# Optimization experiments

Hardware: AMD Instinct MI355X
Metric: run time of the kernel (lower is better)

The kernel has to match this reference:

```python
import jax, jax.numpy as jnp
import numpy as np

EMBD = 256
HEAD = 4
HD = EMBD // HEAD  # 64
EPS = 1e-5


def setup_inputs() -> dict:
    key = jax.random.key(0)
    ks = jax.random.split(key, 12)
    s = lambda fan_in: 1.0 / np.sqrt(fan_in)
    return {
        "x": jax.random.normal(ks[0], (16, 1024, EMBD), dtype=jnp.float32),
        # attention params (stored as [in, out])
        "qkv_w": jax.random.uniform(ks[1], (EMBD, 3 * EMBD), jnp.float32, -s(EMBD), s(EMBD)),
        "qkv_b": jax.random.uniform(ks[2], (3 * EMBD,), jnp.float32, -s(EMBD), s(EMBD)),
        "out_w": jax.random.uniform(ks[3], (EMBD, EMBD), jnp.float32, -s(EMBD), s(EMBD)),
        "out_b": jax.random.uniform(ks[4], (EMBD,), jnp.float32, -s(EMBD), s(EMBD)),
        # MLP params
        "fc_w": jax.random.uniform(ks[5], (EMBD, 4 * EMBD), jnp.float32, -s(EMBD), s(EMBD)),
        "fc_b": jax.random.uniform(ks[6], (4 * EMBD,), jnp.float32, -s(EMBD), s(EMBD)),
        "proj_w": jax.random.uniform(ks[7], (4 * EMBD, EMBD), jnp.float32, -s(4 * EMBD), s(4 * EMBD)),
        "proj_b": jax.random.uniform(ks[8], (EMBD,), jnp.float32, -s(4 * EMBD), s(4 * EMBD)),
        # LayerNorm params
        "ln1_g": jnp.ones((EMBD,), jnp.float32),
        "ln1_b": jnp.zeros((EMBD,), jnp.float32),
        "ln2_g": jnp.ones((EMBD,), jnp.float32),
        "ln2_b": jnp.zeros((EMBD,), jnp.float32),
    }


def layer_norm(x, g, b):
    mu = jnp.mean(x, axis=-1, keepdims=True)
    var = jnp.mean(jnp.square(x - mu), axis=-1, keepdims=True)
    return (x - mu) * jax.lax.rsqrt(var + EPS) * g + b


def block_forward(x, qkv_w, qkv_b, out_w, out_b, fc_w, fc_b, proj_w, proj_b,
                  ln1_g, ln1_b, ln2_g, ln2_b):
    B, S, E = x.shape
    # --- attention branch ---
    h = layer_norm(x, ln1_g, ln1_b)
    qkv = h @ qkv_w + qkv_b                       # [B,S,3E]
    q, k, v = jnp.split(qkv, 3, axis=-1)
    q = q.reshape(B, S, HEAD, HD).transpose(0, 2, 1, 3)  # [B,H,S,D]
    k = k.reshape(B, S, HEAD, HD).transpose(0, 2, 1, 3)
    v = v.reshape(B, S, HEAD, HD).transpose(0, 2, 1, 3)
    att = jnp.einsum('bhqd,bhkd->bhqk', q, k) / jnp.sqrt(jnp.float32(HD))
    causal = jnp.tril(jnp.ones((S, S), dtype=bool))
    att = jnp.where(causal, att, -jnp.inf)
    att = jax.nn.softmax(att, axis=-1)
    o = jnp.einsum('bhqk,bhkd->bhqd', att, v)     # [B,H,S,D]
    o = o.transpose(0, 2, 1, 3).reshape(B, S, E)
    x = x + o @ out_w + out_b
    # --- MLP branch (dropout inactive at eval) ---
    h = layer_norm(x, ln2_g, ln2_b)
    h = jax.nn.relu(h @ fc_w + fc_b)
    x = x + h @ proj_w + proj_b
    return x


def reference(x, qkv_w, qkv_b, out_w, out_b, fc_w, fc_b, proj_w, proj_b,
              ln1_g, ln1_b, ln2_g, ln2_b):
    return block_forward(x, qkv_w, qkv_b, out_w, out_b, fc_w, fc_b,
                         proj_w, proj_b, ln1_g, ln1_b, ln2_g, ln2_b)
```

## Files before the change

### kernel.cpp

```cpp
#include <hip/hip_runtime.h>
#include <cstdint>


using f32x4  = __attribute__((ext_vector_type(4))) float;
using f32x16 = __attribute__((ext_vector_type(16))) float;
using s16x8  = __attribute__((ext_vector_type(8))) short;
using s16x4  = __attribute__((ext_vector_type(4))) short;

__device__ inline short f2bf(float f) {
    union { float f; unsigned u; } v{f};
    unsigned r = (v.u + 0x7FFFu + ((v.u >> 16) & 1u)) >> 16;
    return (short)r;
}

__device__ inline int cvt_pk_bf16(float lo, float hi) {
    int d;
    asm("v_cvt_pk_bf16_f32 %0, %1, %2" : "=v"(d) : "v"(lo), "v"(hi));
    return d;
}
__device__ inline void swap32(int& a, int& b) {
    asm("v_permlane32_swap_b32 %0, %1" : "+v"(a), "+v"(b));
}
__device__ inline void swap16(int& a, int& b) {
    asm("v_permlane16_swap_b32 %0, %1" : "+v"(a), "+v"(b));
}

__device__ inline void gload16(const void* g, void* l) {
    __builtin_amdgcn_global_load_lds(
        (const __attribute__((address_space(1))) void*)g,
        (__attribute__((address_space(3))) void*)l, 16, 0, 0);
}

__global__ __launch_bounds__(256) void prep_kernel(
    const float* __restrict__ qkv_w, const float* __restrict__ out_w,
    const float* __restrict__ fc_w,  const float* __restrict__ proj_w,
    short* __restrict__ wt_qkv, short* __restrict__ wt_out,
    short* __restrict__ wt_fc,  short* __restrict__ wt_proj,
    const float* __restrict__ x, const float* __restrict__ ln1_g,
    const float* __restrict__ ln1_b, short* __restrict__ hout)
{
    __shared__ short T[64][65];
    int id  = blockIdx.x;
    int tid = threadIdx.x;

    if (id < 192) {
        const float* W; short* Wt; int K, N, nt, kt;
        if (id < 48)       { W = qkv_w;  Wt = wt_qkv;  K = 256;  N = 768;  nt = id % 12;        kt = id / 12; }
        else if (id < 64)  { W = out_w;  Wt = wt_out;  K = 256;  N = 256;  nt = (id - 48) & 3;  kt = (id - 48) >> 2; }
        else if (id < 128) { W = fc_w;   Wt = wt_fc;   K = 256;  N = 1024; nt = (id - 64) & 15; kt = (id - 64) >> 4; }
        else               { W = proj_w; Wt = wt_proj; K = 1024; N = 256;  nt = (id - 128) & 3; kt = (id - 128) >> 2; }
        int n0 = nt * 64, k0 = kt * 64;
        int r = tid >> 2, c = (tid & 3) << 4;
        const float* src = W + (size_t)(k0 + r) * N + n0 + c;
#pragma unroll
        for (int u = 0; u < 4; ++u) {
            float4 v = *reinterpret_cast<const float4*>(src + u * 4);
            T[r][c + u * 4 + 0] = f2bf(v.x);
            T[r][c + u * 4 + 1] = f2bf(v.y);
            T[r][c + u * 4 + 2] = f2bf(v.z);
            T[r][c + u * 4 + 3] = f2bf(v.w);
        }
        __syncthreads();
        s16x8 o0, o1;
#pragma unroll
        for (int jj = 0; jj < 8; ++jj) { o0[jj] = T[c + jj][r]; o1[jj] = T[c + 8 + jj][r]; }
        short* dst = Wt + (size_t)(n0 + r) * K + k0 + c;
        *reinterpret_cast<s16x8*>(dst)     = o0;
        *reinterpret_cast<s16x8*>(dst + 8) = o1;
    } else {
        int lane = tid & 63;
        int row  = (id - 192) * 4 + (tid >> 6);
        const float* xr = x + (size_t)row * 256;
        float4 v = *reinterpret_cast<const float4*>(xr + lane * 4);
        float s = v.x + v.y + v.z + v.w;
#pragma unroll
        for (int o2 = 32; o2 >= 1; o2 >>= 1) s += __shfl_xor(s, o2);
        float mu = s * (1.0f / 256.0f);
        float dx = v.x - mu, dy = v.y - mu, dz = v.z - mu, dw = v.w - mu;
        float q = dx * dx + dy * dy + dz * dz + dw * dw;
#pragma unroll
        for (int o2 = 32; o2 >= 1; o2 >>= 1) q += __shfl_xor(q, o2);
        float rstd = rsqrtf(q * (1.0f / 256.0f) + 1e-5f);
        float4 gv = *reinterpret_cast<const float4*>(ln1_g + lane * 4);
        float4 bv = *reinterpret_cast<const float4*>(ln1_b + lane * 4);
        s16x4 ov;
        ov[0] = f2bf(dx * rstd * gv.x + bv.x);
        ov[1] = f2bf(dy * rstd * gv.y + bv.y);
        ov[2] = f2bf(dz * rstd * gv.z + bv.z);
        ov[3] = f2bf(dw * rstd * gv.w + bv.w);
        *reinterpret_cast<s16x4*>(hout + (size_t)row * 256 + lane * 4) = ov;
    }
}

template <int BM>
__global__ __launch_bounds__(256) void qkv_gemm_kernel(const short* __restrict__ A,
                                                       const short* __restrict__ Bt,
                                                       const float* __restrict__ bias,
                                                       short* __restrict__ qkout,
                                                       short* __restrict__ vt,
                                                       int N, int K)
{
    constexpr int MI = BM / 32;
    __shared__ short As[BM * 64];
    __shared__ short Bs[128 * 64];

    int tid = threadIdx.x;
    int l   = tid & 63;
    int w   = tid >> 6;
    int lr  = l & 15;
    int lk8 = (l >> 4) << 3;
    int r4  = (l >> 4) << 2;
    int wr  = w >> 1, wc = w & 1;
    int bn  = blockIdx.x * 128, bm = blockIdx.y * BM;

    int scolS = ((l & 7) << 3) ^ ((l >> 3) << 3);
    int srowA = w * (BM / 4) + (l >> 3);
    int srowB = (w << 5) + (l >> 3);
    const short* pa = A  + (size_t)(bm + srowA) * K + scolS;
    const short* pb = Bt + (size_t)(bn + srowB) * K + scolS;
    short* dstA = As + w * (BM / 4) * 64;
    short* dstB = Bs + (w << 11);

    f32x4 acc[MI][4];
#pragma unroll
    for (int mi = 0; mi < MI; ++mi)
#pragma unroll
        for (int ni = 0; ni < 4; ++ni) acc[mi][ni] = (f32x4){0.f, 0.f, 0.f, 0.f};

    int swz = (lr & 7) << 3;

    for (int k0 = 0; k0 < K; k0 += 64) {
        __syncthreads();
#pragma unroll
        for (int i = 0; i < BM / 32; ++i)
            gload16(pa + (size_t)(i * 8) * K + k0, dstA + (i << 9));
#pragma unroll
        for (int i = 0; i < 4; ++i)
            gload16(pb + (size_t)(i * 8) * K + k0, dstB + (i << 9));
        __syncthreads();

#pragma unroll
        for (int ks = 0; ks < 2; ++ks) {
            s16x8 af[MI], bf[4];
#pragma unroll
            for (int mi = 0; mi < MI; ++mi) {
                int row = wr * (BM / 2) + (mi << 4) + lr;
                af[mi] = *reinterpret_cast<const s16x8*>(
                    &As[(row << 6) + (((ks << 5) + lk8) ^ swz)]);
            }
#pragma unroll
            for (int ni = 0; ni < 4; ++ni) {
                int row = (wc << 6) + (ni << 4) + lr;
                bf[ni] = *reinterpret_cast<const s16x8*>(
                    &Bs[(row << 6) + (((ks << 5) + lk8) ^ swz)]);
            }
            __builtin_amdgcn_s_setprio(1);
#pragma unroll
            for (int mi = 0; mi < MI; ++mi)
#pragma unroll
                for (int ni = 0; ni < 4; ++ni)
                    acc[mi][ni] = __builtin_amdgcn_mfma_f32_16x16x32_bf16(
                        af[mi], bf[ni], acc[mi][ni], 0, 0, 0);
            __builtin_amdgcn_s_setprio(0);
        }
    }

    const float SCQ = 0.125f * 1.44269504088896f;
    float scale = (bn < 256) ? SCQ : 1.0f;

    float bv[4];
#pragma unroll
    for (int ni = 0; ni < 4; ++ni)
        bv[ni] = bias[bn + (wc << 6) + (ni << 4) + lr];

#pragma unroll
    for (int mi = 0; mi < MI; ++mi) {
#pragma unroll
        for (int ni = 0; ni < 4; ++ni) {
            int n = bn + (wc << 6) + (ni << 4) + lr;
#pragma unroll
            for (int r = 0; r < 4; ++r) {
                int m = bm + wr * (BM / 2) + (mi << 4) + r4 + r;
                float v = acc[mi][ni][r] + bv[ni];
                if (bn < 512) {
                    qkout[(size_t)m * 512 + n] = f2bf(v * scale);
                } else {
                    int hh = (n - 512) >> 6, dd = (n - 512) & 63;
                    int bb = m >> 10, ss = m & 1023;
                    vt[(size_t)((((bb << 2) | hh) << 6) | dd) * 1024 + ss] = f2bf(v);
                }
            }
        }
    }
}

template <int RELU, int RES, int OBF16, int BM, int DBUF>
__global__ __launch_bounds__(256) void mgemm_kernel(const short* __restrict__ A,
                                                    const short* __restrict__ Bt,
                                                    const float* __restrict__ bias,
                                                    const float* __restrict__ R,
                                                    void* __restrict__ Cv,
                                                    int N, int K)
{
    constexpr int MI  = BM / 32;
    constexpr int ASZ = BM * 64;
    constexpr int BSZ = 128 * 64;
    __shared__ short As[(1 + DBUF) * ASZ];
    __shared__ short Bs[(1 + DBUF) * BSZ];

    int tid = threadIdx.x;
    int l   = tid & 63;
    int w   = tid >> 6;
    int lr  = l & 15;
    int lk8 = (l >> 4) << 3;
    int r4  = (l >> 4) << 2;
    int wr  = w >> 1, wc = w & 1;
    int bn  = blockIdx.x * 128, bm = blockIdx.y * BM;

    int scolS = ((l & 7) << 3) ^ ((l >> 3) << 3);
    int srowA = w * (BM / 4) + (l >> 3);
    int srowB = (w << 5) + (l >> 3);
    const short* pa = A  + (size_t)(bm + srowA) * K + scolS;
    const short* pb = Bt + (size_t)(bn + srowB) * K + scolS;
    short* dstA = As + w * (BM / 4) * 64;
    short* dstB = Bs + (w << 11);

    f32x4 acc[MI][4];
#pragma unroll
    for (int mi = 0; mi < MI; ++mi)
#pragma unroll
        for (int ni = 0; ni < 4; ++ni) acc[mi][ni] = (f32x4){0.f, 0.f, 0.f, 0.f};

    int swz = (lr & 7) << 3;
    int cur = 0;

    if (DBUF) {
#pragma unroll
        for (int i = 0; i < BM / 32; ++i)
            gload16(pa + (size_t)(i * 8) * K, dstA + (i << 9));
#pragma unroll
        for (int i = 0; i < 4; ++i)
            gload16(pb + (size_t)(i * 8) * K, dstB + (i << 9));
        __syncthreads();
    }

    for (int k0 = 0; k0 < K; k0 += 64) {
        if (DBUF) {
            if (k0 + 64 < K) {
                int nxt = cur ^ 1;
#pragma unroll
                for (int i = 0; i < BM / 32; ++i)
                    gload16(pa + (size_t)(i * 8) * K + k0 + 64, dstA + nxt * ASZ + (i << 9));
#pragma unroll
                for (int i = 0; i < 4; ++i)
                    gload16(pb + (size_t)(i * 8) * K + k0 + 64, dstB + nxt * BSZ + (i << 9));
            }
        } else {
            __syncthreads();
#pragma unroll
            for (int i = 0; i < BM / 32; ++i)
                gload16(pa + (size_t)(i * 8) * K + k0, dstA + (i << 9));
#pragma unroll
            for (int i = 0; i < 4; ++i)
                gload16(pb + (size_t)(i * 8) * K + k0, dstB + (i << 9));
            __syncthreads();
        }
        const short* curA = As + cur * ASZ;
        const short* curB = Bs + cur * BSZ;
#pragma unroll
        for (int ks = 0; ks < 2; ++ks) {
            s16x8 af[MI], bf[4];
#pragma unroll
            for (int mi = 0; mi < MI; ++mi) {
                int row = wr * (BM / 2) + (mi << 4) + lr;
                af[mi] = *reinterpret_cast<const s16x8*>(
                    &curA[(row << 6) + (((ks << 5) + lk8) ^ swz)]);
            }
#pragma unroll
            for (int ni = 0; ni < 4; ++ni) {
                int row = (wc << 6) + (ni << 4) + lr;
                bf[ni] = *reinterpret_cast<const s16x8*>(
                    &curB[(row << 6) + (((ks << 5) + lk8) ^ swz)]);
            }
            __builtin_amdgcn_s_setprio(1);
#pragma unroll
            for (int mi = 0; mi < MI; ++mi)
#pragma unroll
                for (int ni = 0; ni < 4; ++ni)
                    acc[mi][ni] = __builtin_amdgcn_mfma_f32_16x16x32_bf16(
                        af[mi], bf[ni], acc[mi][ni], 0, 0, 0);
            __builtin_amdgcn_s_setprio(0);
        }
        if (DBUF) {
            __syncthreads();
            cur ^= 1;
        }
    }

    float bv[4];
#pragma unroll
    for (int ni = 0; ni < 4; ++ni)
        bv[ni] = bias[bn + (wc << 6) + (ni << 4) + lr];

#pragma unroll
    for (int mi = 0; mi < MI; ++mi) {
#pragma unroll
        for (int ni = 0; ni < 4; ++ni) {
            int n = bn + (wc << 6) + (ni << 4) + lr;
#pragma unroll
            for (int r = 0; r < 4; ++r) {
                int m = bm + wr * (BM / 2) + (mi << 4) + r4 + r;
                float v = acc[mi][ni][r] + bv[ni];
                if (RELU) v = fmaxf(v, 0.0f);
                if (RES)  v += R[(size_t)m * N + n];
                if (OBF16) ((short*)Cv)[(size_t)m * N + n] = f2bf(v);
                else       ((float*)Cv)[(size_t)m * N + n] = v;
            }
        }
    }
}

__global__ __launch_bounds__(256) void oproj_ln_kernel(const short* __restrict__ A,
                                                       const short* __restrict__ Bt,
                                                       const float* __restrict__ bias,
                                                       const float* __restrict__ R,
                                                       float* __restrict__ x1,
                                                       short* __restrict__ h2,
                                                       const float* __restrict__ g,
                                                       const float* __restrict__ bb)
{
    constexpr int ASZ = 64 * 64;
    constexpr int BSZ = 256 * 64;
    __shared__ short As[2 * ASZ];
    __shared__ short Bs[2 * BSZ];

    int tid = threadIdx.x;
    int l   = tid & 63;
    int w   = tid >> 6;
    int lr  = l & 15;
    int lk8 = (l >> 4) << 3;
    int r4  = (l >> 4) << 2;
    int bm  = blockIdx.x * 64;

    int scolS = ((l & 7) << 3) ^ ((l >> 3) << 3);
    const short* pa = A  + (size_t)(bm + (w << 4) + (l >> 3)) * 256 + scolS;
    const short* pb = Bt + (size_t)((w << 6) + (l >> 3)) * 256 + scolS;
    short* dstA = As + (w << 10);
    short* dstB = Bs + (w << 12);

    f32x4 acc[16];
#pragma unroll
    for (int ni = 0; ni < 16; ++ni) acc[ni] = (f32x4){0.f, 0.f, 0.f, 0.f};

    int swz = (lr & 7) << 3;

#pragma unroll
    for (int i = 0; i < 2; ++i)
        gload16(pa + (size_t)(i * 8) * 256, dstA + (i << 9));
#pragma unroll
    for (int i = 0; i < 8; ++i)
        gload16(pb + (size_t)(i * 8) * 256, dstB + (i << 9));
    __syncthreads();

    int cur = 0;
    for (int k0 = 0; k0 < 256; k0 += 64) {
        if (k0 + 64 < 256) {
            int nxt = cur ^ 1;
#pragma unroll
            for (int i = 0; i < 2; ++i)
                gload16(pa + (size_t)(i * 8) * 256 + k0 + 64, dstA + nxt * ASZ + (i << 9));
#pragma unroll
            for (int i = 0; i < 8; ++i)
                gload16(pb + (size_t)(i * 8) * 256 + k0 + 64, dstB + nxt * BSZ + (i << 9));
        }
        const short* curA = As + cur * ASZ;
        const short* curB = Bs + cur * BSZ;
#pragma unroll
        for (int ks = 0; ks < 2; ++ks) {
            int arow = (w << 4) + lr;
            s16x8 af = *reinterpret_cast<const s16x8*>(
                &curA[(arow << 6) + (((ks << 5) + lk8) ^ swz)]);
            __builtin_amdgcn_s_setprio(1);
#pragma unroll
            for (int ni = 0; ni < 16; ++ni) {
                int row = (ni << 4) + lr;
                s16x8 bf = *reinterpret_cast<const s16x8*>(
                    &curB[(row << 6) + (((ks << 5) + lk8) ^ swz)]);
                acc[ni] = __builtin_amdgcn_mfma_f32_16x16x32_bf16(af, bf, acc[ni], 0, 0, 0);
            }
            __builtin_amdgcn_s_setprio(0);
        }
        __syncthreads();
        cur ^= 1;
    }

#pragma unroll
    for (int ni = 0; ni < 16; ++ni) {
        int n = (ni << 4) + lr;
        float bvx = bias[n];
#pragma unroll
        for (int r = 0; r < 4; ++r) {
            int m = bm + (w << 4) + r4 + r;
            acc[ni][r] += bvx + R[(size_t)m * 256 + n];
        }
    }
#pragma unroll
    for (int r = 0; r < 4; ++r) {
        float s = 0.0f;
#pragma unroll
        for (int ni = 0; ni < 16; ++ni) s += acc[ni][r];
        s += __shfl_xor(s, 1); s += __shfl_xor(s, 2);
        s += __shfl_xor(s, 4); s += __shfl_xor(s, 8);
        float mu = s * (1.0f / 256.0f);
        float q = 0.0f;
#pragma unroll
        for (int ni = 0; ni < 16; ++ni) {
            float d = acc[ni][r] - mu;
            q += d * d;
        }
        q += __shfl_xor(q, 1); q += __shfl_xor(q, 2);
        q += __shfl_xor(q, 4); q += __shfl_xor(q, 8);
        float rstd = rsqrtf(q * (1.0f / 256.0f) + 1e-5f);

        int m = bm + (w << 4) + r4 + r;
#pragma unroll
        for (int ni = 0; ni < 16; ++ni) {
            int n = (ni << 4) + lr;
            float v = acc[ni][r];
            x1[(size_t)m * 256 + n] = v;
            h2[(size_t)m * 256 + n] = f2bf((v - mu) * rstd * g[n] + bb[n]);
        }
    }
}

__global__ __launch_bounds__(256, 2) void attn_kernel(const short* __restrict__ qk,
                                                      const short* __restrict__ vt,
                                                      short* __restrict__ o)
{
    constexpr int KSZ = 128 * 64;
    constexpr int VSZ = 64 * 128;
    __shared__ short Ks[2 * KSZ];
    __shared__ short Vs[2 * VSZ];

    int bid  = blockIdx.x;
    int xcd  = bid & 7;
    int j    = bid >> 3;
    int bhg  = j & 7;
    int qidx = j >> 3;
    int qt   = qidx < 4 ? qidx : 11 - qidx;
    int bh   = (bhg << 3) | xcd;
    int b = bh >> 2, h = bh & 3;

    int tid = threadIdx.x;
    int l   = tid & 63;
    int w   = tid >> 6;
    int lq  = l & 31;
    int hg  = l >> 5;

    int krow0 = (w << 3) + (l >> 3);
    int kscol = ((l & 7) << 3) ^ (((l >> 3) & 7) << 3);
    const short* kgp = qk + (size_t)(b * 1024 + krow0) * 512 + 256 + h * 64 + kscol;
    short* dstK = Ks + (w << 3) * 64;
    int vrow0 = (w << 2) + (l >> 4);
    int vscol = ((l & 15) << 3) ^ ((vrow0 & 7) << 3);
    const short* vgp = vt + (size_t)((bh << 6) + vrow0) * 1024 + vscol;
    short* dstV = Vs + (w << 2) * 128;

    const short* qrow = qk + (size_t)(b * 1024 + qt * 128 + (w << 5) + lq) * 512
                        + h * 64 + (hg << 3);
    s16x8 qf[4];
#pragma unroll
    for (int ds = 0; ds < 4; ++ds)
        qf[ds] = *reinterpret_cast<const s16x8*>(qrow + 16 * ds);

#pragma unroll
    for (int i = 0; i < 4; ++i) {
        gload16(kgp + (size_t)(i * 32) * 512, dstK + i * 32 * 64);
        gload16(vgp + (size_t)(i * 16) * 1024, dstV + i * 16 * 128);
    }
    __syncthreads();

    float m = -1e30f, lsum = 0.0f;
    f32x16 oacc[2];
#pragma unroll
    for (int dt = 0; dt < 2; ++dt)
#pragma unroll
        for (int r = 0; r < 16; ++r) oacc[dt][r] = 0.0f;
    int qglob = qt * 128 + (w << 5) + lq;
    int cur = 0;
    int niter = qt + 1;

    for (int kt = 0; kt < niter; ++kt) {
        if (kt + 1 < niter) {
            int nxt = cur ^ 1;
#pragma unroll
            for (int i = 0; i < 4; ++i) {
                gload16(kgp + (size_t)((kt + 1) * 128 + i * 32) * 512,
                        dstK + nxt * KSZ + i * 32 * 64);
                gload16(vgp + (size_t)(i * 16) * 1024 + (kt + 1) * 128,
                        dstV + nxt * VSZ + i * 16 * 128);
            }
        }

        f32x16 sv[4];
#pragma unroll
        for (int jt = 0; jt < 4; ++jt)
#pragma unroll
            for (int r = 0; r < 16; ++r) sv[jt][r] = 0.0f;
        __builtin_amdgcn_s_setprio(1);
#pragma unroll
        for (int ds = 0; ds < 4; ++ds) {
#pragma unroll
            for (int jt = 0; jt < 4; ++jt) {
                int row = jt * 32 + lq;
                s16x8 kf = *reinterpret_cast<const s16x8*>(
                    &Ks[cur * KSZ + (row << 6) + ((16 * ds + (hg << 3)) ^ ((row & 7) << 3))]);
                sv[jt] = __builtin_amdgcn_mfma_f32_32x32x16_bf16(kf, qf[ds], sv[jt], 0, 0, 0);
            }
        }
        __builtin_amdgcn_s_setprio(0);

        if (kt == niter - 1) {
#pragma unroll
            for (int jt = 0; jt < 4; ++jt)
#pragma unroll
                for (int r = 0; r < 16; ++r) {
                    int kg = kt * 128 + jt * 32 + (r & 3) + ((r >> 2) << 3) + (hg << 2);
                    if (kg > qglob) sv[jt][r] = -1e30f;
                }
        }

        float rm = -1e30f;
#pragma unroll
        for (int jt = 0; jt < 4; ++jt)
#pragma unroll
            for (int r = 0; r < 16; ++r) rm = fmaxf(rm, sv[jt][r]);
        rm = fmaxf(rm, __shfl_xor(rm, 32));
        bool big = __any(rm > m + 8.0f);
        float fct = 1.0f;
        if (big) {
            float mn = fmaxf(m, rm);
            fct = exp2f(m - mn);
            m = mn;
        }
        float ps = 0.0f;
#pragma unroll
        for (int jt = 0; jt < 4; ++jt)
#pragma unroll
            for (int r = 0; r < 16; ++r) {
                float p = exp2f(sv[jt][r] - m);
                sv[jt][r] = p;
                ps += p;
            }
        ps += __shfl_xor(ps, 32);
        lsum = lsum * fct + ps;

        if (big) {
#pragma unroll
            for (int r = 0; r < 16; ++r) {
                float f = __shfl(fct, (r & 3) + ((r >> 2) << 3) + (hg << 2));
                oacc[0][r] *= f;
                oacc[1][r] *= f;
            }
        }

#pragma unroll
        for (int jt = 0; jt < 4; ++jt) {
            int x0 = cvt_pk_bf16(sv[jt][0],  sv[jt][1]);
            int x1v = cvt_pk_bf16(sv[jt][2],  sv[jt][3]);
            int y0 = cvt_pk_bf16(sv[jt][4],  sv[jt][5]);
            int y1 = cvt_pk_bf16(sv[jt][6],  sv[jt][7]);
            int z0 = cvt_pk_bf16(sv[jt][8],  sv[jt][9]);
            int z1 = cvt_pk_bf16(sv[jt][10], sv[jt][11]);
            int w0 = cvt_pk_bf16(sv[jt][12], sv[jt][13]);
            int w1 = cvt_pk_bf16(sv[jt][14], sv[jt][15]);
            swap32(x0, y0); swap32(x1v, y1);
            swap32(z0, w0); swap32(z1, w1);
            union { int i[4]; s16x8 v; } fA, fB;
            fA.i[0] = x0; fA.i[1] = x1v; fA.i[2] = y0; fA.i[3] = y1;
            fB.i[0] = z0; fB.i[1] = z1;  fB.i[2] = w0; fB.i[3] = w1;
            __builtin_amdgcn_s_setprio(1);
#pragma unroll
            for (int dt = 0; dt < 2; ++dt) {
                int row = dt * 32 + lq;
                int rs  = (row & 7) << 3;
                s16x8 vfA = *reinterpret_cast<const s16x8*>(
                    &Vs[cur * VSZ + (row << 7) + ((16 * (2 * jt)     + (hg << 3)) ^ rs)]);
                oacc[dt] = __builtin_amdgcn_mfma_f32_32x32x16_bf16(fA.v, vfA, oacc[dt], 0, 0, 0);
                s16x8 vfB = *reinterpret_cast<const s16x8*>(
                    &Vs[cur * VSZ + (row << 7) + ((16 * (2 * jt + 1) + (hg << 3)) ^ rs)]);
                oacc[dt] = __builtin_amdgcn_mfma_f32_32x32x16_bf16(fB.v, vfB, oacc[dt], 0, 0, 0);
            }
            __builtin_amdgcn_s_setprio(0);
        }

        if (kt + 1 < niter) {
            __syncthreads();
            cur ^= 1;
        }
    }

#pragma unroll
    for (int r = 0; r < 16; ++r) {
        int qr  = (r & 3) + ((r >> 2) << 3) + (hg << 2);
        float lv  = __shfl(lsum, qr);
        float inv = 1.0f / lv;
        int q = qt * 128 + (w << 5) + qr;
        short* orow = o + (size_t)(b * 1024 + q) * 256 + h * 64;
        orow[lq]      = f2bf(oacc[0][r] * inv);
        orow[32 + lq] = f2bf(oacc[1][r] * inv);
    }
}

extern "C" void kernel_launch(void* const* d_in, const int* in_sizes, int n_in,
                              void* d_out, int out_size, void* d_ws, size_t ws_size,
                              hipStream_t stream)
{
    const float* x      = (const float*)d_in[0];
    const float* qkv_w  = (const float*)d_in[1];
    const float* qkv_b  = (const float*)d_in[2];
    const float* out_w  = (const float*)d_in[3];
    const float* out_b  = (const float*)d_in[4];
    const float* fc_w   = (const float*)d_in[5];
    const float* fc_b   = (const float*)d_in[6];
    const float* proj_w = (const float*)d_in[7];
    const float* proj_b = (const float*)d_in[8];
    const float* ln1_g  = (const float*)d_in[9];
    const float* ln1_b  = (const float*)d_in[10];
    const float* ln2_g  = (const float*)d_in[11];
    const float* ln2_b  = (const float*)d_in[12];
    float* out = (float*)d_out;

    short* ws = (short*)d_ws;
    short* wt_qkv  = ws;
    short* wt_out  = ws + 196608;
    short* wt_fc   = ws + 262144;
    short* wt_proj = ws + 524288;
    short* bufA    = ws + 786432;
    short* qk_buf  = ws + 4980736;
    short* vt_buf  = ws + 13369344;
    short* h3_buf  = ws + 4980736;

    dim3 blk(256);

    prep_kernel<<<dim3(4288), blk, 0, stream>>>(
        qkv_w, out_w, fc_w, proj_w, wt_qkv, wt_out, wt_fc, wt_proj,
        x, ln1_g, ln1_b, bufA);
    qkv_gemm_kernel<128><<<dim3(6, 128), blk, 0, stream>>>(
        bufA, wt_qkv, qkv_b, qk_buf, vt_buf, 768, 256);
    attn_kernel<<<dim3(512), blk, 0, stream>>>(qk_buf, vt_buf, bufA);
    oproj_ln_kernel<<<dim3(256), blk, 0, stream>>>(
        bufA, wt_out, out_b, x, out, bufA, ln2_g, ln2_b);
    mgemm_kernel<1, 0, 1, 128, 0><<<dim3(8, 128), blk, 0, stream>>>(
        bufA, wt_fc, fc_b, nullptr, h3_buf, 1024, 256);
    mgemm_kernel<0, 1, 0, 64, 1><<<dim3(2, 256), blk, 0, stream>>>(
        h3_buf, wt_proj, proj_b, out, out, 256, 1024);
}
```

Before: 120.2 us.

## Load K and V fragments directly from global memory in attention kernel

Removes the double-buffered LDS staging of K and V tiles and the per-iteration block barrier in the attention kernel. Each wave now reads its K and V MFMA fragments straight from global memory, relying on L1/L2 caching for reuse across the four waves that share the same tiles. This eliminates LDS traffic and __syncthreads, but gives up the explicit prefetch overlap and turns shared tile reuse into redundant global/cache reads with latency exposed before the MFMAs.

```diff
diff --git a/kernel.cpp b/kernel.cpp
--- a/kernel.cpp
+++ b/kernel.cpp
@@ -437,11 +437,6 @@
                                                       const short* __restrict__ vt,
                                                       short* __restrict__ o)
 {
-    constexpr int KSZ = 128 * 64;
-    constexpr int VSZ = 64 * 128;
-    __shared__ short Ks[2 * KSZ];
-    __shared__ short Vs[2 * VSZ];
-
     int bid  = blockIdx.x;
     int xcd  = bid & 7;
     int j    = bid >> 3;
@@ -457,14 +452,8 @@
     int lq  = l & 31;
     int hg  = l >> 5;
 
-    int krow0 = (w << 3) + (l >> 3);
-    int kscol = ((l & 7) << 3) ^ (((l >> 3) & 7) << 3);
-    const short* kgp = qk + (size_t)(b * 1024 + krow0) * 512 + 256 + h * 64 + kscol;
-    short* dstK = Ks + (w << 3) * 64;
-    int vrow0 = (w << 2) + (l >> 4);
-    int vscol = ((l & 15) << 3) ^ ((vrow0 & 7) << 3);
-    const short* vgp = vt + (size_t)((bh << 6) + vrow0) * 1024 + vscol;
-    short* dstV = Vs + (w << 2) * 128;
+    const short* kbase = qk + (size_t)(b * 1024) * 512 + 256 + h * 64;
+    const short* vbase = vt + (size_t)(bh << 6) * 1024;
 
     const short* qrow = qk + (size_t)(b * 1024 + qt * 128 + (w << 5) + lq) * 512
                         + h * 64 + (hg << 3);
@@ -473,13 +462,6 @@
     for (int ds = 0; ds < 4; ++ds)
         qf[ds] = *reinterpret_cast<const s16x8*>(qrow + 16 * ds);
 
-#pragma unroll
-    for (int i = 0; i < 4; ++i) {
-        gload16(kgp + (size_t)(i * 32) * 512, dstK + i * 32 * 64);
-        gload16(vgp + (size_t)(i * 16) * 1024, dstV + i * 16 * 128);
-    }
-    __syncthreads();
-
     float m = -1e30f, lsum = 0.0f;
     f32x16 oacc[2];
 #pragma unroll
@@ -487,38 +469,27 @@
 #pragma unroll
         for (int r = 0; r < 16; ++r) oacc[dt][r] = 0.0f;
     int qglob = qt * 128 + (w << 5) + lq;
-    int cur = 0;
     int niter = qt + 1;
 
     for (int kt = 0; kt < niter; ++kt) {
-        if (kt + 1 < niter) {
-            int nxt = cur ^ 1;
-#pragma unroll
-            for (int i = 0; i < 4; ++i) {
-                gload16(kgp + (size_t)((kt + 1) * 128 + i * 32) * 512,
-                        dstK + nxt * KSZ + i * 32 * 64);
-                gload16(vgp + (size_t)(i * 16) * 1024 + (kt + 1) * 128,
-                        dstV + nxt * VSZ + i * 16 * 128);
-            }
-        }
-
         f32x16 sv[4];
 #pragma unroll
         for (int jt = 0; jt < 4; ++jt)
 #pragma unroll
             for (int r = 0; r < 16; ++r) sv[jt][r] = 0.0f;
-        __builtin_amdgcn_s_setprio(1);
-#pragma unroll
-        for (int ds = 0; ds < 4; ++ds) {
-#pragma unroll
-            for (int jt = 0; jt < 4; ++jt) {
-                int row = jt * 32 + lq;
-                s16x8 kf = *reinterpret_cast<const s16x8*>(
-                    &Ks[cur * KSZ + (row << 6) + ((16 * ds + (hg << 3)) ^ ((row & 7) << 3))]);
-                sv[jt] = __builtin_amdgcn_mfma_f32_32x32x16_bf16(kf, qf[ds], sv[jt], 0, 0, 0);
-            }
-        }
-        __builtin_amdgcn_s_setprio(0);
+#pragma unroll
+        for (int jt = 0; jt < 4; ++jt) {
+            const short* krow = kbase + (size_t)(kt * 128 + jt * 32 + lq) * 512 + (hg << 3);
+            s16x8 kf[4];
+#pragma unroll
+            for (int ds = 0; ds < 4; ++ds)
+                kf[ds] = *reinterpret_cast<const s16x8*>(krow + 16 * ds);
+            __builtin_amdgcn_s_setprio(1);
+#pragma unroll
+            for (int ds = 0; ds < 4; ++ds)
+                sv[jt] = __builtin_amdgcn_mfma_f32_32x32x16_bf16(kf[ds], qf[ds], sv[jt], 0, 0, 0);
+            __builtin_amdgcn_s_setprio(0);
+        }
 
         if (kt == niter - 1) {
 #pragma unroll
@@ -579,24 +550,17 @@
             union { int i[4]; s16x8 v; } fA, fB;
             fA.i[0] = x0; fA.i[1] = x1v; fA.i[2] = y0; fA.i[3] = y1;
             fB.i[0] = z0; fB.i[1] = z1;  fB.i[2] = w0; fB.i[3] = w1;
-            __builtin_amdgcn_s_setprio(1);
 #pragma unroll
             for (int dt = 0; dt < 2; ++dt) {
-                int row = dt * 32 + lq;
-                int rs  = (row & 7) << 3;
-                s16x8 vfA = *reinterpret_cast<const s16x8*>(
-                    &Vs[cur * VSZ + (row << 7) + ((16 * (2 * jt)     + (hg << 3)) ^ rs)]);
+                const short* vrow = vbase + (size_t)(dt * 32 + lq) * 1024
+                                    + kt * 128 + (hg << 3);
+                s16x8 vfA = *reinterpret_cast<const s16x8*>(vrow + 16 * (2 * jt));
+                s16x8 vfB = *reinterpret_cast<const s16x8*>(vrow + 16 * (2 * jt + 1));
+                __builtin_amdgcn_s_setprio(1);
                 oacc[dt] = __builtin_amdgcn_mfma_f32_32x32x16_bf16(fA.v, vfA, oacc[dt], 0, 0, 0);
-                s16x8 vfB = *reinterpret_cast<const s16x8*>(
-                    &Vs[cur * VSZ + (row << 7) + ((16 * (2 * jt + 1) + (hg << 3)) ^ rs)]);
                 oacc[dt] = __builtin_amdgcn_mfma_f32_32x32x16_bf16(fB.v, vfB, oacc[dt], 0, 0, 0);
-            }
-            __builtin_amdgcn_s_setprio(0);
-        }
-
-        if (kt + 1 < niter) {
-            __syncthreads();
-            cur ^= 1;
+                __builtin_amdgcn_s_setprio(0);
+            }
         }
     }
 
```

New measurement: 137.3 us. 1.14x slower.
